# Optimization experiments

Hardware: AMD Instinct MI355X
Metric: run time of the kernel (lower is better)

Reference implementation:

```python
import jax, jax.numpy as jnp
import numpy as np

B, N, DIM = 2, 4096, 512
HEADS, HEAD_DIM = 8, 64
INNER = HEADS * HEAD_DIM


def setup_inputs() -> dict:
    key = jax.random.key(0)
    k1, k2, k3 = jax.random.split(key, 3)
    x = jax.random.normal(k1, (B, N, DIM), dtype=jnp.float32)
    w_qkv = jax.random.normal(k2, (DIM, 3 * INNER), dtype=jnp.float32) * (DIM ** -0.5)
    temperature = jnp.asarray(np.log(HEAD_DIM ** -0.5), dtype=jnp.float32)
    w_out = jax.random.normal(k3, (INNER, DIM), dtype=jnp.float32) * (INNER ** -0.5)
    b_out = jnp.zeros((DIM,), dtype=jnp.float32)
    return {"x": x, "w_qkv": w_qkv, "temperature": temperature, "w_out": w_out, "b_out": b_out}


def reference(x, w_qkv, temperature, w_out, b_out):
    b, n, _ = x.shape
    qkv = x @ w_qkv                                   # (B, N, 3*inner)
    q, k, v = jnp.split(qkv, 3, axis=-1)
    # Faithful to original: raw reshape (NOT transpose) into (B, H, N, d)
    q = q.reshape(b, HEADS, n, HEAD_DIM)
    k = k.reshape(b, HEADS, n, HEAD_DIM)
    v = v.reshape(b, HEADS, n, HEAD_DIM)
    scores = jnp.einsum('bhnd,bhmd->bhnm', q, k) * jnp.exp(temperature)
    mask = jnp.eye(n, dtype=bool)                     # diagonal self-mask
    mask_value = jnp.finfo(scores.dtype).min
    scores = jnp.where(mask, mask_value, scores)
    attn = jax.nn.softmax(scores, axis=-1)
    out = jnp.einsum('bhnm,bhmd->bhnd', attn, v)      # (B, H, N, d)
    # Faithful to original: raw reshape (NOT transpose) back to (B, N, H*d)
    out = out.reshape(b, n, HEADS * HEAD_DIM)
    return out @ w_out + b_out                        # dropout inactive at inference
```

## Files before the change

kernel.cpp:

```cpp
#include <hip/hip_runtime.h>


typedef __bf16 bf16;
typedef __bf16 bf16x8 __attribute__((ext_vector_type(8)));
typedef __bf16 bf16x4 __attribute__((ext_vector_type(4)));
typedef __bf16 bf16x2 __attribute__((ext_vector_type(2)));
typedef float  f32x4  __attribute__((ext_vector_type(4)));
typedef float  f32x16 __attribute__((ext_vector_type(16)));
typedef unsigned u32x4 __attribute__((ext_vector_type(4)));

#define MFMA_BF16(a, b, c)   __builtin_amdgcn_mfma_f32_16x16x32_bf16((a), (b), (c), 0, 0, 0)
#define MFMA32_BF16(a, b, c) __builtin_amdgcn_mfma_f32_32x32x16_bf16((a), (b), (c), 0, 0, 0)

__device__ __forceinline__ void gld_lds16(void* lds, const void* g) {
  __builtin_amdgcn_global_load_lds(
      (const __attribute__((address_space(1))) void*)g,
      (__attribute__((address_space(3))) void*)lds, 16, 0, 0);
}

__device__ __forceinline__ unsigned pkbf(float a, float b) {
  bf16x2 t; t[0] = (bf16)a; t[1] = (bf16)b;
  return __builtin_bit_cast(unsigned, t);
}


__global__ void cast4_kernel(const float* __restrict__ in, bf16* __restrict__ out, int n4) {
  int i = blockIdx.x * 256 + threadIdx.x;
  if (i >= n4) return;
  float4 v = ((const float4*)in)[i];
  bf16x4 o;
  o[0] = (bf16)v.x; o[1] = (bf16)v.y; o[2] = (bf16)v.z; o[3] = (bf16)v.w;
  *(bf16x4*)(out + 4 * i) = o;
}

__global__ void wtrans_kernel(const float* __restrict__ in, bf16* __restrict__ out, int C) {
  __shared__ float tile[64 * 65];
  const int t = threadIdx.x;
  const int c0 = blockIdx.x * 64, r0 = blockIdx.y * 64;
#pragma unroll
  for (int p = 0; p < 16; p++) {
    int idx = p * 256 + t, r = idx >> 6, c = idx & 63;
    tile[r * 65 + c] = in[(r0 + r) * C + c0 + c];
  }
  __syncthreads();
#pragma unroll
  for (int p = 0; p < 16; p++) {
    int idx = p * 256 + t, c = idx >> 6, r = idx & 63;
    out[(size_t)(c0 + c) * 512 + r0 + r] = (bf16)tile[r * 65 + c];
  }
}

__global__ void vtrans_kernel(const bf16* __restrict__ V, bf16* __restrict__ Vt) {
  __shared__ bf16 tile[64 * 65];
  const int t = threadIdx.x;
  const size_t base = (size_t)blockIdx.y << 18;
  const int n0 = blockIdx.x * 64;
#pragma unroll
  for (int p = 0; p < 16; p++) {
    int idx = p * 256 + t, r = idx >> 6, c = idx & 63;
    tile[r * 65 + c] = V[base + (size_t)(n0 + r) * 64 + c];
  }
  __syncthreads();
#pragma unroll
  for (int p = 0; p < 16; p++) {
    int idx = p * 256 + t, d = idx >> 6, n = idx & 63;
    Vt[base + (size_t)d * 4096 + n0 + n] = tile[n * 65 + d];
  }
}


template<int EPI, int WNT>
__global__ __launch_bounds__(256) void gemm_bt(
    const bf16* __restrict__ A, const bf16* __restrict__ Bt,
    bf16* __restrict__ oQ, bf16* __restrict__ oK, bf16* __restrict__ oV,
    float* __restrict__ oC, const float* __restrict__ bias,
    const float* __restrict__ temp)
{
  __shared__ bf16 As[128 * 32];
  __shared__ bf16 Bs[WNT * 32 * 32];

  const int t    = threadIdx.x;
  const int lane = t & 63;
  const int w    = t >> 6;
  const int mm   = lane & 15;
  const int q    = lane >> 4;
  const int wm   = w >> 1, wn = w & 1;
  const int m0   = blockIdx.y * 128;
  const int n0   = blockIdx.x * (WNT * 32);

  const int srow = t >> 2, sch = t & 3;
  const int gch  = sch ^ ((srow >> 1) & 3);
  const bf16* Ab = A  + (m0 + srow) * 512 + gch * 8;
  const bf16* Bb = Bt + (n0 + srow) * 512 + gch * 8;
  bf16* Asl = As + t * 8;
  bf16* Bsl = Bs + t * 8;

  const int fslot = (q ^ ((mm >> 1) & 3)) * 8;

  const f32x4 zero4 = {0.f, 0.f, 0.f, 0.f};
  f32x4 acc[4][WNT];
#pragma unroll
  for (int i = 0; i < 4; i++)
#pragma unroll
    for (int j = 0; j < WNT; j++) acc[i][j] = zero4;

  for (int k0 = 0; k0 < 512; k0 += 32) {
    __syncthreads();
    gld_lds16(Asl,        Ab + k0);
    gld_lds16(Asl + 2048, Ab + 64 * 512 + k0);
    gld_lds16(Bsl,        Bb + k0);
    if (WNT == 4) gld_lds16(Bsl + 2048, Bb + 64 * 512 + k0);
    __syncthreads();

    bf16x8 af[4], bfv[WNT];
#pragma unroll
    for (int i = 0; i < 4; i++)
      af[i] = *(const bf16x8*)(As + (wm * 64 + i * 16 + mm) * 32 + fslot);
#pragma unroll
    for (int j = 0; j < WNT; j++)
      bfv[j] = *(const bf16x8*)(Bs + (wn * (WNT * 16) + j * 16 + mm) * 32 + fslot);

#pragma unroll
    for (int i = 0; i < 4; i++)
#pragma unroll
      for (int j = 0; j < WNT; j++)
        acc[i][j] = MFMA_BF16(af[i], bfv[j], acc[i][j]);
  }

  if (EPI == 0) {
    const float scale = __expf(temp[0]) * 1.44269504088896f;
#pragma unroll
    for (int i = 0; i < 4; i++) {
      const int row = m0 + wm * 64 + i * 16 + q * 4;
#pragma unroll
      for (int j = 0; j < WNT; j++) {
        const int col = n0 + wn * (WNT * 16) + j * 16 + mm;
        bf16* dst; int c2; float s;
        if (col < 512)       { dst = oQ; c2 = col;        s = scale; }
        else if (col < 1024) { dst = oK; c2 = col - 512;  s = 1.0f;  }
        else                 { dst = oV; c2 = col - 1024; s = 1.0f;  }
#pragma unroll
        for (int r = 0; r < 4; r++)
          dst[(size_t)(row + r) * 512 + c2] = (bf16)(acc[i][j][r] * s);
      }
    }
  } else {
#pragma unroll
    for (int i = 0; i < 4; i++) {
      const int row = m0 + wm * 64 + i * 16 + q * 4;
#pragma unroll
      for (int j = 0; j < WNT; j++) {
        const int col = n0 + wn * (WNT * 16) + j * 16 + mm;
        const float b = bias[col];
#pragma unroll
        for (int r = 0; r < 4; r++)
          oC[(size_t)(row + r) * 512 + col] = acc[i][j][r] + b;
      }
    }
  }
}


template<int SPLIT>
__global__ __launch_bounds__(256, 4) void attn_kernel(
    const bf16* __restrict__ Q, const bf16* __restrict__ Kb,
    const bf16* __restrict__ Vt, bf16* __restrict__ O,
    float* __restrict__ Opart, float* __restrict__ Lpart)
{
  __shared__ bf16 Ks[2][64 * 64];
  __shared__ bf16 Vs[2][64 * 64];
  __shared__ float rsum[4][32];

  const int t    = threadIdx.x;
  const int lane = t & 63;
  const int w    = t >> 6;
  const int c32  = lane & 31;
  const int h    = lane >> 5;
  const int pxa  = (lane ^ 32) << 2;
  const int bh   = blockIdx.y;
  const int q0   = blockIdx.x * 128;
  const int z    = blockIdx.z;
  const size_t hb = (size_t)bh << 18;
  const bf16* Qh = Q  + hb;
  const bf16* Kh = Kb + hb;
  const bf16* Vh = Vt + hb;
  const int q0w  = q0 + w * 32;

  int tlo, tn;
  if (SPLIT == 1)      { tlo = 0;      tn = 64; }
  else                 { tlo = z * 32; tn = 32; }

  bf16x8 qf[4];
#pragma unroll
  for (int s = 0; s < 4; s++)
    qf[s] = *(const bf16x8*)(Qh + (size_t)(q0w + c32) * 64 + s * 16 + h * 8);

  f32x16 o[2];
#pragma unroll
  for (int dt = 0; dt < 2; dt++)
#pragma unroll
    for (int r = 0; r < 16; r++) o[dt][r] = 0.f;
  float lacc = 0.f;

  const int r0 = t >> 3, c0 = t & 7;
  const int g0 = c0 ^ (r0 & 7);
  const bf16* Kg = Kh + (size_t)r0 * 64 + g0 * 8;
  const bf16* Vg = Vh + (size_t)r0 * 4096 + g0 * 8;

  const int dbase = q0w & ~63;
  const int kthalf = (q0w >> 5) & 1;

  {
    const int kv0 = tlo * 64;
    gld_lds16(&Ks[0][t * 8],        Kg + (size_t)kv0 * 64);
    gld_lds16(&Ks[0][t * 8] + 2048, Kg + (size_t)(kv0 + 32) * 64);
    gld_lds16(&Vs[0][t * 8],        Vg + kv0);
    gld_lds16(&Vs[0][t * 8] + 2048, Vg + (size_t)32 * 4096 + kv0);
  }

  for (int it = 0; it < tn; it++) {
    const int cur = it & 1;
    if (it + 1 < tn) {
      const int kv1 = (tlo + it + 1) * 64;
      bf16* Kn = &Ks[cur ^ 1][t * 8];
      bf16* Vn = &Vs[cur ^ 1][t * 8];
      gld_lds16(Kn,        Kg + (size_t)kv1 * 64);
      gld_lds16(Kn + 2048, Kg + (size_t)(kv1 + 32) * 64);
      gld_lds16(Vn,        Vg + kv1);
      gld_lds16(Vn + 2048, Vg + (size_t)32 * 4096 + kv1);
      __asm__ volatile("s_waitcnt vmcnt(4)" ::: "memory");
    } else {
      __asm__ volatile("s_waitcnt vmcnt(0)" ::: "memory");
    }
    __builtin_amdgcn_s_barrier();
    __asm__ volatile("" ::: "memory");

    const int kv0 = (tlo + it) * 64;
    const bool diag = (kv0 == dbase);
    const bf16* Kc = Ks[cur];
    const bf16* Vc = Vs[cur];

#pragma unroll
    for (int kt = 0; kt < 2; kt++) {
      bf16x8 kf[4];
      const int kr = kt * 32 + c32;
#pragma unroll
      for (int s = 0; s < 4; s++)
        kf[s] = *(const bf16x8*)(Kc + kr * 64 + (((s << 1) | h) ^ (kr & 7)) * 8);

      f32x16 sv;
#pragma unroll
      for (int r = 0; r < 16; r++) sv[r] = 0.f;
      __builtin_amdgcn_s_setprio(1);
#pragma unroll
      for (int s = 0; s < 4; s++)
        sv = MFMA32_BF16(kf[s], qf[s], sv);
      __builtin_amdgcn_s_setprio(0);

      float pp[16];
#pragma unroll
      for (int r = 0; r < 16; r++) pp[r] = __builtin_amdgcn_exp2f(sv[r]);
      if (diag && kt == kthalf) {
#pragma unroll
        for (int r = 0; r < 16; r++)
          if (c32 == ((r & 3) + ((r >> 2) << 3) + (h << 2))) pp[r] = 0.f;
      }
      float s8[8];
#pragma unroll
      for (int r = 0; r < 8; r++) s8[r] = pp[r] + pp[r + 8];
      float s4[4];
#pragma unroll
      for (int r = 0; r < 4; r++) s4[r] = s8[r] + s8[r + 4];
      lacc += (s4[0] + s4[1]) + (s4[2] + s4[3]);

      bf16x8 pa[2];
#pragma unroll
      for (int s2 = 0; s2 < 2; s2++) {
        const int b = s2 * 8;
        unsigned wa = pkbf(pp[b + 0], pp[b + 1]);
        unsigned wc = pkbf(pp[b + 2], pp[b + 3]);
        unsigned wb = pkbf(pp[b + 4], pp[b + 5]);
        unsigned wd = pkbf(pp[b + 6], pp[b + 7]);
        unsigned r1 = (unsigned)__builtin_amdgcn_ds_bpermute(pxa, (int)(h ? wa : wb));
        unsigned r2 = (unsigned)__builtin_amdgcn_ds_bpermute(pxa, (int)(h ? wc : wd));
        u32x4 wv;
        wv[0] = h ? r1 : wa;
        wv[1] = h ? r2 : wc;
        wv[2] = h ? wb : r1;
        wv[3] = h ? wd : r2;
        pa[s2] = __builtin_bit_cast(bf16x8, wv);
      }

#pragma unroll
      for (int s2 = 0; s2 < 2; s2++) {
        bf16x8 vf[2];
#pragma unroll
        for (int dt = 0; dt < 2; dt++) {
          const int d = dt * 32 + c32;
          vf[dt] = *(const bf16x8*)(Vc + d * 64 + (((((kt << 1) | s2) << 1) | h) ^ (d & 7)) * 8);
        }
        __builtin_amdgcn_s_setprio(1);
#pragma unroll
        for (int dt = 0; dt < 2; dt++)
          o[dt] = MFMA32_BF16(pa[s2], vf[dt], o[dt]);
        __builtin_amdgcn_s_setprio(0);
      }
    }
    __asm__ volatile("" ::: "memory");
    __builtin_amdgcn_s_barrier();
  }

  const int pb = __builtin_amdgcn_ds_bpermute(pxa, __builtin_bit_cast(int, lacc));
  const float tot = lacc + __builtin_bit_cast(float, pb);

  if (SPLIT == 1) {
    bf16* Oh = O + hb;
    if (h == 0) rsum[w][c32] = tot;
    __asm__ volatile("s_waitcnt lgkmcnt(0)" ::: "memory");
#pragma unroll
    for (int r = 0; r < 16; r++) {
      const int row = (r & 3) + ((r >> 2) << 3) + (h << 2);
      const float rinv = 1.0f / rsum[w][row];
#pragma unroll
      for (int dt = 0; dt < 2; dt++)
        Oh[(size_t)(q0w + row) * 64 + dt * 32 + c32] = (bf16)(o[dt][r] * rinv);
    }
  } else {
    float* Op = Opart + ((size_t)z << 22) + hb;
    float* Lp = Lpart + (z << 16) + (bh << 12);
    if (h == 0) Lp[q0w + c32] = tot;
#pragma unroll
    for (int r = 0; r < 16; r++) {
      const int row = (r & 3) + ((r >> 2) << 3) + (h << 2);
#pragma unroll
      for (int dt = 0; dt < 2; dt++)
        Op[(size_t)(q0w + row) * 64 + dt * 32 + c32] = o[dt][r];
    }
  }
}

template<int SPLIT>
__global__ void merge_kernel(const float* __restrict__ Op, const float* __restrict__ Lp,
                             bf16* __restrict__ Ob) {
  const int g = blockIdx.x * 256 + threadIdx.x;
  const int f = g * 4;
  const int row = f >> 6;
  float l = 0.f;
  float4 a = {0.f, 0.f, 0.f, 0.f};
#pragma unroll
  for (int zz = 0; zz < SPLIT; zz++) {
    l += Lp[(zz << 16) + row];
    const float4 b = *(const float4*)(Op + ((size_t)zz << 22) + f);
    a.x += b.x; a.y += b.y; a.z += b.z; a.w += b.w;
  }
  const float rinv = 1.0f / l;
  bf16x4 o;
  o[0] = (bf16)(a.x * rinv);
  o[1] = (bf16)(a.y * rinv);
  o[2] = (bf16)(a.z * rinv);
  o[3] = (bf16)(a.w * rinv);
  *(bf16x4*)(Ob + f) = o;
}


extern "C" void kernel_launch(void* const* d_in, const int* in_sizes, int n_in,
                              void* d_out, int out_size, void* d_ws, size_t ws_size,
                              hipStream_t stream) {
  const float* x      = (const float*)d_in[0];
  const float* w_qkv  = (const float*)d_in[1];
  const float* temp   = (const float*)d_in[2];
  const float* w_out  = (const float*)d_in[3];
  const float* b_out  = (const float*)d_in[4];
  float* out          = (float*)d_out;

  char* ws = (char*)d_ws;
  bf16*  Xb    = (bf16*)(ws);
  bf16*  Wt    = (bf16*)(ws + (size_t)(8u  << 20));
  bf16*  Qb    = (bf16*)(ws + (size_t)(10u << 20));
  bf16*  Kb    = (bf16*)(ws + (size_t)(18u << 20));
  bf16*  Vb    = (bf16*)(ws + (size_t)(26u << 20));
  bf16*  Vtb   = (bf16*)(ws + (size_t)(34u << 20));
  bf16*  Ob    = (bf16*)(ws + (size_t)(42u << 20));
  bf16*  Wot   = (bf16*)(ws + (size_t)(50u << 20));
  float* Lpart = (float*)(ws + (size_t)(51u << 20));
  float* Opart = (float*)(ws + (size_t)(52u << 20));

  const int split = (ws_size >= ((size_t)86u << 20)) ? 2 : 1;

  cast4_kernel<<<4096, 256, 0, stream>>>(x, Xb, (8192 * 512) / 4);
  wtrans_kernel<<<dim3(24, 8), 256, 0, stream>>>(w_qkv, Wt, 1536);
  wtrans_kernel<<<dim3(8, 8), 256, 0, stream>>>(w_out, Wot, 512);

  gemm_bt<0, 4><<<dim3(12, 64), 256, 0, stream>>>(Xb, Wt, Qb, Kb, Vb, nullptr, nullptr, temp);

  vtrans_kernel<<<dim3(64, 16), 256, 0, stream>>>(Vb, Vtb);

  if (split == 2) {
    attn_kernel<2><<<dim3(32, 16, 2), 256, 0, stream>>>(Qb, Kb, Vtb, nullptr, Opart, Lpart);
    merge_kernel<2><<<4096, 256, 0, stream>>>(Opart, Lpart, Ob);
  } else {
    attn_kernel<1><<<dim3(32, 16, 1), 256, 0, stream>>>(Qb, Kb, Vtb, Ob, nullptr, nullptr);
  }

  gemm_bt<1, 2><<<dim3(8, 64), 256, 0, stream>>>(Ob, Wot, nullptr, nullptr, nullptr, out, b_out, nullptr);
}
```

Baseline: 211.5 us.

## Rotate KV tile order per block and batch both QK MFMA groups before softmax

```diff
diff --git a/kernel.cpp b/kernel.cpp
--- a/kernel.cpp
+++ b/kernel.cpp
@@ -189,6 +189,8 @@
   int tlo, tn;
   if (SPLIT == 1)      { tlo = 0;      tn = 64; }
   else                 { tlo = z * 32; tn = 32; }
+  const int tmask = tn - 1;
+  const int rot = (blockIdx.x * 5 + bh * 11 + z * 16) & tmask;
 
   bf16x8 qf[4];
 #pragma unroll
@@ -211,7 +213,7 @@
   const int kthalf = (q0w >> 5) & 1;
 
   {
-    const int kv0 = tlo * 64;
+    const int kv0 = (tlo + rot) * 64;
     gld_lds16(&Ks[0][t * 8],        Kg + (size_t)kv0 * 64);
     gld_lds16(&Ks[0][t * 8] + 2048, Kg + (size_t)(kv0 + 32) * 64);
     gld_lds16(&Vs[0][t * 8],        Vg + kv0);
@@ -220,51 +222,66 @@
 
   for (int it = 0; it < tn; it++) {
     const int cur = it & 1;
-    if (it + 1 < tn) {
-      const int kv1 = (tlo + it + 1) * 64;
+    {
+      const int kvn = (tlo + ((it + 1 + rot) & tmask)) * 64;
       bf16* Kn = &Ks[cur ^ 1][t * 8];
       bf16* Vn = &Vs[cur ^ 1][t * 8];
-      gld_lds16(Kn,        Kg + (size_t)kv1 * 64);
-      gld_lds16(Kn + 2048, Kg + (size_t)(kv1 + 32) * 64);
-      gld_lds16(Vn,        Vg + kv1);
-      gld_lds16(Vn + 2048, Vg + (size_t)32 * 4096 + kv1);
-      __asm__ volatile("s_waitcnt vmcnt(4)" ::: "memory");
-    } else {
-      __asm__ volatile("s_waitcnt vmcnt(0)" ::: "memory");
-    }
+      gld_lds16(Kn,        Kg + (size_t)kvn * 64);
+      gld_lds16(Kn + 2048, Kg + (size_t)(kvn + 32) * 64);
+      gld_lds16(Vn,        Vg + kvn);
+      gld_lds16(Vn + 2048, Vg + (size_t)32 * 4096 + kvn);
+    }
+    __asm__ volatile("s_waitcnt vmcnt(4)" ::: "memory");
     __builtin_amdgcn_s_barrier();
     __asm__ volatile("" ::: "memory");
 
-    const int kv0 = (tlo + it) * 64;
+    const int kv0 = (tlo + ((it + rot) & tmask)) * 64;
     const bool diag = (kv0 == dbase);
     const bf16* Kc = Ks[cur];
     const bf16* Vc = Vs[cur];
 
-#pragma unroll
-    for (int kt = 0; kt < 2; kt++) {
+    f32x16 sv0, sv1;
+#pragma unroll
+    for (int r = 0; r < 16; r++) { sv0[r] = 0.f; sv1[r] = 0.f; }
+    {
       bf16x8 kf[4];
-      const int kr = kt * 32 + c32;
+#pragma unroll
+      for (int s = 0; s < 4; s++)
+        kf[s] = *(const bf16x8*)(Kc + c32 * 64 + (((s << 1) | h) ^ (c32 & 7)) * 8);
+#pragma unroll
+      for (int s = 0; s < 4; s++)
+        sv0 = MFMA32_BF16(kf[s], qf[s], sv0);
+    }
+    {
+      const int kr = 32 + c32;
+      bf16x8 kf[4];
 #pragma unroll
       for (int s = 0; s < 4; s++)
         kf[s] = *(const bf16x8*)(Kc + kr * 64 + (((s << 1) | h) ^ (kr & 7)) * 8);
-
-      f32x16 sv;
-#pragma unroll
-      for (int r = 0; r < 16; r++) sv[r] = 0.f;
-      __builtin_amdgcn_s_setprio(1);
 #pragma unroll
       for (int s = 0; s < 4; s++)
-        sv = MFMA32_BF16(kf[s], qf[s], sv);
-      __builtin_amdgcn_s_setprio(0);
-
+        sv1 = MFMA32_BF16(kf[s], qf[s], sv1);
+    }
+
+    if (diag) {
+      if (kthalf == 0) {
+#pragma unroll
+        for (int r = 0; r < 16; r++)
+          if (c32 == ((r & 3) + ((r >> 2) << 3) + (h << 2))) sv0[r] = -1e30f;
+      } else {
+#pragma unroll
+        for (int r = 0; r < 16; r++)
+          if (c32 == ((r & 3) + ((r >> 2) << 3) + (h << 2))) sv1[r] = -1e30f;
+      }
+    }
+
+    bf16x8 pa00, pa01, pa10, pa11;
+#pragma unroll
+    for (int kt = 0; kt < 2; kt++) {
       float pp[16];
 #pragma unroll
-      for (int r = 0; r < 16; r++) pp[r] = __builtin_amdgcn_exp2f(sv[r]);
-      if (diag && kt == kthalf) {
-#pragma unroll
-        for (int r = 0; r < 16; r++)
-          if (c32 == ((r & 3) + ((r >> 2) << 3) + (h << 2))) pp[r] = 0.f;
-      }
+      for (int r = 0; r < 16; r++)
+        pp[r] = __builtin_amdgcn_exp2f(kt ? sv1[r] : sv0[r]);
       float s8[8];
 #pragma unroll
       for (int r = 0; r < 8; r++) s8[r] = pp[r] + pp[r + 8];
@@ -273,7 +290,6 @@
       for (int r = 0; r < 4; r++) s4[r] = s8[r] + s8[r + 4];
       lacc += (s4[0] + s4[1]) + (s4[2] + s4[3]);
 
-      bf16x8 pa[2];
 #pragma unroll
       for (int s2 = 0; s2 < 2; s2++) {
         const int b = s2 * 8;
@@ -288,24 +304,28 @@
         wv[1] = h ? r2 : wc;
         wv[2] = h ? wb : r1;
         wv[3] = h ? wd : r2;
-        pa[s2] = __builtin_bit_cast(bf16x8, wv);
+        bf16x8 pa = __builtin_bit_cast(bf16x8, wv);
+        if (kt == 0) { if (s2 == 0) pa00 = pa; else pa01 = pa; }
+        else         { if (s2 == 0) pa10 = pa; else pa11 = pa; }
       }
-
+    }
+
+#pragma unroll
+    for (int kt = 0; kt < 2; kt++)
 #pragma unroll
       for (int s2 = 0; s2 < 2; s2++) {
+        const bf16x8 pa = kt ? (s2 ? pa11 : pa10) : (s2 ? pa01 : pa00);
         bf16x8 vf[2];
 #pragma unroll
         for (int dt = 0; dt < 2; dt++) {
           const int d = dt * 32 + c32;
           vf[dt] = *(const bf16x8*)(Vc + d * 64 + (((((kt << 1) | s2) << 1) | h) ^ (d & 7)) * 8);
         }
-        __builtin_amdgcn_s_setprio(1);
 #pragma unroll
         for (int dt = 0; dt < 2; dt++)
-          o[dt] = MFMA32_BF16(pa[s2], vf[dt], o[dt]);
-        __builtin_amdgcn_s_setprio(0);
+          o[dt] = MFMA32_BF16(pa, vf[dt], o[dt]);
       }
-    }
+
     __asm__ volatile("" ::: "memory");
     __builtin_amdgcn_s_barrier();
   }
```

Result: slower. 219.9 us (+4.0%).
